# Performance work log

Hardware: AMD Instinct MI355X
Metric: run time of the kernel (lower is better)

The kernel has to match this reference:

```python
import jax, jax.numpy as jnp
import numpy as np

HIDDEN = 1024
HEADS = 16
HEAD_DIM = 64
B, S = 2, 2048
SCALE = 1.0 / np.sqrt(HEAD_DIM)
NEG = -1e9


def setup_inputs() -> dict:
    key = jax.random.key(0)
    k1, k2, k3, k4, k5 = jax.random.split(key, 5)
    hidden_states = jax.random.normal(k1, (B, S, HIDDEN), dtype=jnp.float32)
    # causal additive mask, broadcast over heads: [B, 1, S, S]
    causal = jnp.where(jnp.tril(jnp.ones((S, S), dtype=bool)), 0.0, NEG).astype(jnp.float32)
    attention_mask = jnp.broadcast_to(causal[None, None], (B, 1, S, S))
    std = 1.0 / np.sqrt(HIDDEN)
    Wq = jax.random.normal(k2, (HIDDEN, HEADS * HEAD_DIM), dtype=jnp.float32) * std
    Wk = jax.random.normal(k3, (HIDDEN, HEADS * HEAD_DIM), dtype=jnp.float32) * std
    Wv = jax.random.normal(k4, (HIDDEN, HEADS * HEAD_DIM), dtype=jnp.float32) * std
    Wo = jax.random.normal(k5, (HEADS * HEAD_DIM, HIDDEN), dtype=jnp.float32) * std
    return {"hidden_states": hidden_states, "attention_mask": attention_mask,
            "Wq": Wq, "Wk": Wk, "Wv": Wv, "Wo": Wo}


def reference(hidden_states, attention_mask, Wq, Wk, Wv, Wo):
    b, s, _ = hidden_states.shape
    # projections (eval mode: dropouts are identity)
    q = (hidden_states @ Wq).reshape(b, s, HEADS, HEAD_DIM).transpose(0, 2, 1, 3)  # [B,H,S,D]
    k = (hidden_states @ Wk).reshape(b, s, HEADS, HEAD_DIM).transpose(0, 2, 1, 3)
    v = (hidden_states @ Wv).reshape(b, s, HEADS, HEAD_DIM).transpose(0, 2, 1, 3)
    scores = jnp.einsum('bhqd,bhkd->bhqk', q, k) * SCALE + attention_mask  # [B,H,S,S]
    probs = jax.nn.softmax(scores, axis=-1)
    out = jnp.einsum('bhqk,bhkd->bhqd', probs, v)  # [B,H,S,D]
    out = out.transpose(0, 2, 1, 3).reshape(b, s, HEADS * HEAD_DIM)
    return out @ Wo  # [B,S,HIDDEN]
```

## Files before the change

### kernel.cpp

```cpp
#include <hip/hip_runtime.h>

typedef unsigned short u16;
typedef unsigned int u32;
typedef __bf16 bf16x8 __attribute__((ext_vector_type(8)));
typedef float f32x4 __attribute__((ext_vector_type(4)));

#define MFMA(a, b, c) __builtin_amdgcn_mfma_f32_16x16x32_bf16(a, b, c, 0, 0, 0)

#define GLD16(gsrc, ldst)                                                          \
  __builtin_amdgcn_global_load_lds(                                                \
      (const __attribute__((address_space(1))) void*)(gsrc),                       \
      (__attribute__((address_space(3))) void*)(ldst), 16, 0, 0)

#if __has_builtin(__builtin_amdgcn_exp2f)
#define EXP2(x) __builtin_amdgcn_exp2f(x)
#else
#define EXP2(x) exp2f(x)
#endif

__device__ __forceinline__ u16 f2bf(float f) {
  return __builtin_bit_cast(u16, (__bf16)f);
}

__device__ __forceinline__ u32 pk2(float a, float b) {
  __bf16 x = (__bf16)a, y = (__bf16)b;
  return (u32)__builtin_bit_cast(u16, x) | ((u32)__builtin_bit_cast(u16, y) << 16);
}

__device__ __forceinline__ float bf2f(u16 u) {
  return __builtin_bit_cast(float, ((u32)u) << 16);
}

__global__ __launch_bounds__(256) void k_prep(
    const float* __restrict__ X, const float* __restrict__ Wq,
    const float* __restrict__ Wk, const float* __restrict__ Wv,
    const float* __restrict__ Wo, u16* __restrict__ Xb,
    u16* __restrict__ Wt, u16* __restrict__ Wot) {
  __shared__ u16 t[32][33];
  int bid = blockIdx.x;
  if (bid < 2048) {
    int i = bid * 256 + threadIdx.x;
    const float4* p = (const float4*)X + (size_t)i * 2;
    float4 a = p[0], b = p[1];
    uint4 o;
    o.x = pk2(a.x, a.y);
    o.y = pk2(a.z, a.w);
    o.z = pk2(b.x, b.y);
    o.w = pk2(b.z, b.w);
    *(uint4*)(Xb + (size_t)i * 8) = o;
    return;
  }
  bid -= 2048;
  const int k0 = (bid & 31) * 32, n0 = (bid >> 5) * 32;
  const int x = threadIdx.x & 31, y = threadIdx.x >> 5;
  const float* src = (n0 < 1024) ? Wq : (n0 < 2048) ? Wk : (n0 < 3072) ? Wv : Wo;
  const int ncol = n0 & 1023;
#pragma unroll
  for (int rr = 0; rr < 4; ++rr) {
    int kl = y + rr * 8;
    t[x][kl] = f2bf(src[(size_t)(k0 + kl) * 1024 + ncol + x]);
  }
  __syncthreads();
  u16* dst = (n0 < 3072) ? (Wt + (size_t)n0 * 1024) : (Wot + (size_t)(n0 - 3072) * 1024);
#pragma unroll
  for (int rr = 0; rr < 4; ++rr) {
    int nl = y + rr * 8;
    dst[(size_t)nl * 1024 + k0 + x] = t[nl][x];
  }
}


__global__ __launch_bounds__(256) void k_gemm_qkv(const u16* __restrict__ A_,
                                                  const u16* __restrict__ Bt,
                                                  u16* __restrict__ Q,
                                                  u16* __restrict__ K,
                                                  u16* __restrict__ Vt) {
  __shared__ __align__(16) u16 As[2][128 * 32];
  __shared__ __align__(16) u16 Bs[2][128 * 32];
  const int tid = threadIdx.x;
  const int w = tid >> 6, l = tid & 63;
  const int lr = l & 15, lg = l >> 4;
  const int lin = blockIdx.y * 24 + blockIdx.x;
  const int swz = (lin & 7) * 96 + (lin >> 3);
  const int tM = (swz / 24) * 128, tN = (swz % 24) * 128;
  const int wr = w >> 1, wc = w & 1;
  const int bufsel = tN >> 10;

  const int srow = l >> 2;
  const int scol = (((l & 3) ^ ((l >> 3) & 3)) << 3);
  const u16* Ag = A_ + (size_t)(tM + srow) * 1024 + scol;
  const u16* Bg = Bt + (size_t)(tN + srow) * 1024 + scol;
  const int rs = (lr >> 1) & 3;

#define STAGE_QKV(buf, kk)                                                   \
  {                                                                          \
    GLD16(Ag + (size_t)(w * 16) * 1024 + (kk), &As[buf][(w * 16) * 32]);     \
    GLD16(Ag + (size_t)(64 + w * 16) * 1024 + (kk), &As[buf][(64 + w * 16) * 32]); \
    GLD16(Bg + (size_t)(w * 16) * 1024 + (kk), &Bs[buf][(w * 16) * 32]);     \
    GLD16(Bg + (size_t)(64 + w * 16) * 1024 + (kk), &Bs[buf][(64 + w * 16) * 32]); \
  }

  f32x4 acc[4][4] = {};
  STAGE_QKV(0, 0)
  __syncthreads();
  int cur = 0;

  if (bufsel < 2) {
    for (int t = 0; t < 32; ++t) {
      if (t < 31) STAGE_QKV(cur ^ 1, (t + 1) * 32)
      const u16* Ac = &As[cur][0];
      const u16* Bc = &Bs[cur][0];
      bf16x8 a[4], b[4];
#pragma unroll
      for (int m = 0; m < 4; ++m)
        a[m] = *(const bf16x8*)(Ac + (wr * 64 + m * 16 + lr) * 32 + ((lg ^ rs) << 3));
#pragma unroll
      for (int n = 0; n < 4; ++n)
        b[n] = *(const bf16x8*)(Bc + (wc * 64 + n * 16 + lr) * 32 + ((lg ^ rs) << 3));
#pragma unroll
      for (int m = 0; m < 4; ++m)
#pragma unroll
        for (int n = 0; n < 4; ++n) acc[m][n] = MFMA(b[n], a[m], acc[m][n]);
      __syncthreads();
      cur ^= 1;
    }
    u16* dst = bufsel ? K : Q;
    const float sc = bufsel ? 1.0f : 0.180336880111124f;
#pragma unroll
    for (int m = 0; m < 4; ++m) {
      int s = tM + wr * 64 + m * 16 + lr;
      int b_ = s >> 11, sr2 = s & 2047;
#pragma unroll
      for (int n = 0; n < 4; ++n) {
        int c2 = (tN + wc * 64 + n * 16 + lg * 4) & 1023;
        int h = c2 >> 6, d = c2 & 63;
        uint2 val;
        val.x = pk2(acc[m][n][0] * sc, acc[m][n][1] * sc);
        val.y = pk2(acc[m][n][2] * sc, acc[m][n][3] * sc);
        *(uint2*)(dst + ((size_t)(b_ * 16 + h) * 2048 + sr2) * 64 + d) = val;
      }
    }
  } else {
    for (int t = 0; t < 32; ++t) {
      if (t < 31) STAGE_QKV(cur ^ 1, (t + 1) * 32)
      const u16* Ac = &As[cur][0];
      const u16* Bc = &Bs[cur][0];
      bf16x8 a[4], b[4];
#pragma unroll
      for (int m = 0; m < 4; ++m)
        a[m] = *(const bf16x8*)(Ac + (wr * 64 + m * 16 + lr) * 32 + ((lg ^ rs) << 3));
#pragma unroll
      for (int n = 0; n < 4; ++n)
        b[n] = *(const bf16x8*)(Bc + (wc * 64 + n * 16 + lr) * 32 + ((lg ^ rs) << 3));
#pragma unroll
      for (int m = 0; m < 4; ++m)
#pragma unroll
        for (int n = 0; n < 4; ++n) acc[m][n] = MFMA(a[m], b[n], acc[m][n]);
      __syncthreads();
      cur ^= 1;
    }
#pragma unroll
    for (int m = 0; m < 4; ++m) {
      int r0 = tM + wr * 64 + m * 16 + lg * 4;
      int b_ = r0 >> 11, s0 = r0 & 2047;
#pragma unroll
      for (int n = 0; n < 4; ++n) {
        int c2 = (tN + wc * 64 + n * 16 + lr) & 1023;
        int h = c2 >> 6, d = c2 & 63;
        uint2 val;
        val.x = pk2(acc[m][n][0], acc[m][n][1]);
        val.y = pk2(acc[m][n][2], acc[m][n][3]);
        *(uint2*)(Vt + ((size_t)(b_ * 16 + h) * 64 + d) * 2048 + s0) = val;
      }
    }
  }
#undef STAGE_QKV
}

__global__ __launch_bounds__(256, 4) void k_attn(const u16* __restrict__ Q,
                                                 const u16* __restrict__ Kg,
                                                 const u16* __restrict__ Vtg,
                                                 u16* __restrict__ AO,
                                                 u16* __restrict__ PO,
                                                 float* __restrict__ ML) {
  __shared__ __align__(16) u16 Ks[2][64 * 64];
  __shared__ __align__(16) u16 Vs[2][64 * 64];
  __shared__ __align__(16) u16 Ps[4][16 * 64];
  const int tid = threadIdx.x;
  const int w = tid >> 6, l = tid & 63;
  const int lr = l & 15, lg = l >> 4;

  const int idx = blockIdx.x;
  const int bh = idx & 31;
  const int g = idx >> 5;
  int qt, c0;
  if (g < 16) { qt = 16 + g; c0 = 0; }
  else if (g < 32) { qt = 31 - (g - 16); c0 = 1; }
  else { qt = 15 - (g - 32); c0 = 0; }
  const int nkt = (qt < 16) ? (qt + 1) : (c0 == 0 ? 16 : qt - 15);
  const bool hasdiag = (qt < 16) || (c0 == 1);
  const int q0 = qt * 64;

  const u16* Qp = Q + (size_t)bh * 2048 * 64;
  const u16* Kp = Kg + (size_t)bh * 2048 * 64;
  const u16* Vp = Vtg + (size_t)bh * 64 * 2048;

  const int qrow = q0 + w * 16 + lr;
  bf16x8 qa0 = *(const bf16x8*)(Qp + (size_t)qrow * 64 + lg * 8);
  bf16x8 qa1 = *(const bf16x8*)(Qp + (size_t)qrow * 64 + 32 + lg * 8);

  f32x4 oacc[4] = {};
  float m_run = -1e30f, l_run = 0.f;

  const int srow = l >> 3;
  const int scol = ((l & 7) ^ srow) * 8;
  const int sw = (lr & 7) << 3;

  const u16* kptr = Kp + ((size_t)c0 * 1024 + srow) * 64 + scol;
  const u16* vptr = Vp + (size_t)srow * 2048 + c0 * 1024 + scol;

#pragma unroll
  for (int j = 0; j < 2; ++j) {
    int base = j * 32 + w * 8;
    GLD16(kptr + base * 64, &Ks[0][base * 64]);
    GLD16(vptr + (size_t)base * 2048, &Vs[0][base * 64]);
  }
  kptr += 4096;
  vptr += 64;
  __syncthreads();

  int cur = 0;

#define ATTN_TILE(DOPRE, DOMASK)                                                   \
  {                                                                                \
    if (DOPRE) {                                                                   \
      _Pragma("unroll") for (int j = 0; j < 2; ++j) {                              \
        int base = j * 32 + w * 8;                                                 \
        GLD16(kptr + base * 64, &Ks[cur ^ 1][base * 64]);                          \
        GLD16(vptr + (size_t)base * 2048, &Vs[cur ^ 1][base * 64]);                \
      }                                                                            \
      kptr += 4096;                                                                \
      vptr += 64;                                                                  \
    }                                                                              \
    f32x4 st[4];                                                                   \
    __builtin_amdgcn_s_setprio(1);                                                 \
    _Pragma("unroll") for (int n = 0; n < 4; ++n) {                                \
      const u16* kr = &Ks[cur][(n * 16 + lr) * 64];                                \
      bf16x8 kb0 = *(const bf16x8*)(kr + ((lg << 3) ^ sw));                        \
      bf16x8 kb1 = *(const bf16x8*)(kr + (((4 + lg) << 3) ^ sw));                  \
      f32x4 z = {0.f, 0.f, 0.f, 0.f};                                              \
      z = MFMA(kb0, qa0, z);                                                       \
      z = MFMA(kb1, qa1, z);                                                       \
      st[n] = z;                                                                   \
    }                                                                              \
    __builtin_amdgcn_s_setprio(0);                                                 \
    float mx = -1e30f;                                                             \
    _Pragma("unroll") for (int n = 0; n < 4; ++n)                                  \
        _Pragma("unroll") for (int j = 0; j < 4; ++j) {                            \
      float s = st[n][j];                                                          \
      if (DOMASK && (n * 16 + lg * 4 + j) > (w * 16 + lr)) s = -1e30f;             \
      st[n][j] = s;                                                                \
      mx = fmaxf(mx, s);                                                           \
    }                                                                              \
    mx = fmaxf(mx, __shfl_xor(mx, 16, 64));                                        \
    mx = fmaxf(mx, __shfl_xor(mx, 32, 64));                                        \
    const bool grow = __any(mx > m_run + 8.0f);               \
    float mnew = grow ? fmaxf(m_run, mx) : m_run;                                  \
    float rsum = 0.f;                                                              \
    _Pragma("unroll") for (int n = 0; n < 4; ++n)                                  \
        _Pragma("unroll") for (int j = 0; j < 4; ++j) {                            \
      float p = EXP2(st[n][j] - mnew);                                             \
      st[n][j] = p;                                                                \
      rsum += p;                                                                   \
    }                                                                              \
    rsum += __shfl_xor(rsum, 16, 64);                                              \
    rsum += __shfl_xor(rsum, 32, 64);                                              \
    if (grow) {                                                                    \
      float fsc = EXP2(m_run - mnew);                                              \
      l_run = l_run * fsc + rsum;                                                  \
      m_run = mnew;                                                                \
      _Pragma("unroll") for (int n = 0; n < 4; ++n)                                \
          _Pragma("unroll") for (int j = 0; j < 4; ++j) oacc[n][j] *= fsc;         \
    } else {                                                                       \
      l_run += rsum;                                                               \
    }                                                                              \
    u16* pb = &Ps[w][0];                                                           \
    _Pragma("unroll") for (int n = 0; n < 4; ++n) {                                \
      int slot = n * 2 + (lg >> 1);                                                \
      int off = lr * 64 + ((slot ^ (lr & 7)) << 3) + (lg & 1) * 4;                 \
      uint2 val;                                                                   \
      val.x = pk2(st[n][0], st[n][1]);                                             \
      val.y = pk2(st[n][2], st[n][3]);                                             \
      *(uint2*)(pb + off) = val;                                                   \
    }                                                                              \
    bf16x8 pa0 = *(const bf16x8*)(pb + lr * 64 + ((lg << 3) ^ sw));                \
    bf16x8 pa1 = *(const bf16x8*)(pb + lr * 64 + (((4 + lg) << 3) ^ sw));          \
    __builtin_amdgcn_s_setprio(1);                                                 \
    _Pragma("unroll") for (int n = 0; n < 4; ++n) {                                \
      const u16* vr = &Vs[cur][(n * 16 + lr) * 64];                                \
      bf16x8 vb0 = *(const bf16x8*)(vr + ((lg << 3) ^ sw));                        \
      bf16x8 vb1 = *(const bf16x8*)(vr + (((4 + lg) << 3) ^ sw));                  \
      oacc[n] = MFMA(vb0, pa0, oacc[n]);                                           \
      oacc[n] = MFMA(vb1, pa1, oacc[n]);                                           \
    }                                                                              \
    __builtin_amdgcn_s_setprio(0);                                                 \
  }

  for (int it = 0; it < nkt - 1; ++it) {
    ATTN_TILE(true, false);
    __syncthreads();
    cur ^= 1;
  }
  if (hasdiag) {
    ATTN_TILE(false, true);
  } else {
    ATTN_TILE(false, false);
  }
#undef ATTN_TILE

  if (qt < 16) {
    const int b_ = bh >> 4, h = bh & 15;
    const float linv = 1.0f / l_run;
    const int s = q0 + w * 16 + lr;
    u16* dst = AO + ((size_t)(b_ * 2048 + s)) * 1024 + h * 64 + lg * 4;
#pragma unroll
    for (int n = 0; n < 4; ++n) {
      uint2 val;
      val.x = pk2(oacc[n][0] * linv, oacc[n][1] * linv);
      val.y = pk2(oacc[n][2] * linv, oacc[n][3] * linv);
      *(uint2*)(dst + n * 16) = val;
    }
  } else {
    const int p = (bh * 16 + (qt - 16)) * 2 + c0;
    u16* po = PO + (size_t)p * 4096 + (size_t)(w * 16 + lr) * 64 + lg * 4;
#pragma unroll
    for (int n = 0; n < 4; ++n) {
      uint2 val;
      val.x = pk2(oacc[n][0], oacc[n][1]);
      val.y = pk2(oacc[n][2], oacc[n][3]);
      *(uint2*)(po + n * 16) = val;
    }
    if (lg == 0) {
      ML[(size_t)p * 128 + (w * 16 + lr)] = m_run;
      ML[(size_t)p * 128 + 64 + (w * 16 + lr)] = l_run;
    }
  }
}

__global__ __launch_bounds__(256) void k_combine(const u16* __restrict__ PO,
                                                 const float* __restrict__ ML,
                                                 u16* __restrict__ AO) {
  const int blk = blockIdx.x;
  const int bh = blk >> 4, qt = 16 + (blk & 15);
  const int row = threadIdx.x >> 2;
  const int dseg = (threadIdx.x & 3) * 16;
  const size_t p0 = (size_t)blk * 2;
  const float m0 = ML[p0 * 128 + row], l0 = ML[p0 * 128 + 64 + row];
  const float m1 = ML[p0 * 128 + 128 + row], l1 = ML[p0 * 128 + 192 + row];
  const float M = fmaxf(m0, m1);
  float w0 = EXP2(m0 - M), w1 = EXP2(m1 - M);
  const float inv = 1.0f / (l0 * w0 + l1 * w1);
  w0 *= inv;
  w1 *= inv;
  const u16* o0 = PO + p0 * 4096 + (size_t)row * 64 + dseg;
  const u16* o1 = o0 + 4096;
  const int b_ = bh >> 4, h = bh & 15;
  u16* dst = AO + ((size_t)(b_ * 2048 + qt * 64 + row)) * 1024 + h * 64 + dseg;
#pragma unroll
  for (int half = 0; half < 2; ++half) {
    uint4 a = *(const uint4*)(o0 + half * 8);
    uint4 b = *(const uint4*)(o1 + half * 8);
    u32 aw[4] = {a.x, a.y, a.z, a.w};
    u32 bw[4] = {b.x, b.y, b.z, b.w};
    uint4 o;
    u32 ow[4];
#pragma unroll
    for (int i = 0; i < 4; ++i) {
      float r0 = bf2f((u16)(aw[i] & 0xffffu)) * w0 + bf2f((u16)(bw[i] & 0xffffu)) * w1;
      float r1 = bf2f((u16)(aw[i] >> 16)) * w0 + bf2f((u16)(bw[i] >> 16)) * w1;
      ow[i] = pk2(r0, r1);
    }
    o.x = ow[0]; o.y = ow[1]; o.z = ow[2]; o.w = ow[3];
    *(uint4*)(dst + half * 8) = o;
  }
}

__global__ __launch_bounds__(256) void k_gemm_out(const u16* __restrict__ A_,
                                                  const u16* __restrict__ Bt,
                                                  float* __restrict__ out) {
  __shared__ __align__(16) u16 As[2][128 * 32];
  __shared__ __align__(16) u16 Bs[2][64 * 32];
  const int tid = threadIdx.x;
  const int w = tid >> 6, l = tid & 63;
  const int lr = l & 15, lg = l >> 4;
  const int lin = blockIdx.y * 16 + blockIdx.x;
  const int swz = (lin & 7) * 64 + (lin >> 3);
  const int tM = (swz / 16) * 128, tN = (swz % 16) * 64;

  const int srow = l >> 2;
  const int scol = (((l & 3) ^ ((l >> 3) & 3)) << 3);
  const u16* Ag = A_ + (size_t)(tM + srow) * 1024 + scol;
  const u16* Bg = Bt + (size_t)(tN + srow) * 1024 + scol;
  const int rs = (lr >> 1) & 3;

#define STAGE_OUT(buf, kk)                                                   \
  {                                                                          \
    GLD16(Ag + (size_t)(w * 16) * 1024 + (kk), &As[buf][(w * 16) * 32]);     \
    GLD16(Ag + (size_t)(64 + w * 16) * 1024 + (kk), &As[buf][(64 + w * 16) * 32]); \
    GLD16(Bg + (size_t)(w * 16) * 1024 + (kk), &Bs[buf][(w * 16) * 32]);     \
  }

  f32x4 acc[2][4] = {};
  STAGE_OUT(0, 0)
  __syncthreads();
  int cur = 0;
  for (int t = 0; t < 32; ++t) {
    if (t < 31) STAGE_OUT(cur ^ 1, (t + 1) * 32)
    const u16* Ac = &As[cur][0];
    const u16* Bc = &Bs[cur][0];
    bf16x8 a[2], b[4];
#pragma unroll
    for (int m = 0; m < 2; ++m)
      a[m] = *(const bf16x8*)(Ac + (w * 32 + m * 16 + lr) * 32 + ((lg ^ rs) << 3));
#pragma unroll
    for (int n = 0; n < 4; ++n)
      b[n] = *(const bf16x8*)(Bc + (n * 16 + lr) * 32 + ((lg ^ rs) << 3));
#pragma unroll
    for (int m = 0; m < 2; ++m)
#pragma unroll
      for (int n = 0; n < 4; ++n) acc[m][n] = MFMA(b[n], a[m], acc[m][n]);
    __syncthreads();
    cur ^= 1;
  }
#undef STAGE_OUT

#pragma unroll
  for (int m = 0; m < 2; ++m) {
    int s = tM + w * 32 + m * 16 + lr;
#pragma unroll
    for (int n = 0; n < 4; ++n) {
      int c = tN + n * 16 + lg * 4;
      float4 v;
      v.x = acc[m][n][0];
      v.y = acc[m][n][1];
      v.z = acc[m][n][2];
      v.w = acc[m][n][3];
      *(float4*)(out + (size_t)s * 1024 + c) = v;
    }
  }
}

extern "C" void kernel_launch(void* const* d_in, const int* in_sizes, int n_in,
                              void* d_out, int out_size, void* d_ws, size_t ws_size,
                              hipStream_t stream) {
  const float* X = (const float*)d_in[0];
  const float* Wq = (const float*)d_in[2];
  const float* Wk = (const float*)d_in[3];
  const float* Wv = (const float*)d_in[4];
  const float* Wo = (const float*)d_in[5];
  float* out = (float*)d_out;

  char* ws = (char*)d_ws;
  if (ws_size < (size_t)48 * 1024 * 1024) return;
  u16* Xb  = (u16*)(ws);
  u16* Wt  = (u16*)(ws + 8388608);
  u16* Wot = (u16*)(ws + 14680064);
  u16* Q   = (u16*)(ws + 16777216);
  u16* K   = (u16*)(ws + 25165824);
  u16* Vt  = (u16*)(ws + 33554432);
  u16* AO  = (u16*)(ws + 41943040);
  u16*   PO = (u16*)(ws);
  float* ML = (float*)(ws + 8388608);

  k_prep<<<6144, 256, 0, stream>>>(X, Wq, Wk, Wv, Wo, Xb, Wt, Wot);
  k_gemm_qkv<<<dim3(24, 32), 256, 0, stream>>>(Xb, Wt, Q, K, Vt);
  k_attn<<<1536, 256, 0, stream>>>(Q, K, Vt, AO, PO, ML);
  k_combine<<<512, 256, 0, stream>>>(PO, ML, AO);
  k_gemm_out<<<dim3(16, 32), 256, 0, stream>>>(AO, Wot, out);
}
```

Measured before the change: 117.3 us.

## Halve attention KV tile to 32 keys to raise occupancy to six waves

Shrinks the K/V LDS tiles in the attention kernel from 64 keys to 32 and doubles the number of KV iterations. This lowers shared-memory use and registers per block so the launch bound can rise to 6 blocks per CU for better latency hiding. The LDS swizzles and P-tile layout are reworked to match, and the causal mask is now applied to the last two tiles using absolute positions. In exchange there are twice as many barriers and softmax rescale steps, and less MFMA work per iteration. The last two tiles are always masked, even for blocks that have no diagonal tile.

```diff
diff --git a/kernel.cpp b/kernel.cpp
--- a/kernel.cpp
+++ b/kernel.cpp
@@ -177,15 +177,15 @@
 #undef STAGE_QKV
 }
 
-__global__ __launch_bounds__(256, 4) void k_attn(const u16* __restrict__ Q,
+__global__ __launch_bounds__(256, 6) void k_attn(const u16* __restrict__ Q,
                                                  const u16* __restrict__ Kg,
                                                  const u16* __restrict__ Vtg,
                                                  u16* __restrict__ AO,
                                                  u16* __restrict__ PO,
                                                  float* __restrict__ ML) {
-  __shared__ __align__(16) u16 Ks[2][64 * 64];
-  __shared__ __align__(16) u16 Vs[2][64 * 64];
-  __shared__ __align__(16) u16 Ps[4][16 * 64];
+  __shared__ __align__(16) u16 Ks[2][32 * 64];
+  __shared__ __align__(16) u16 Vs[2][64 * 32];
+  __shared__ __align__(16) u16 Ps[4][16 * 32];
   const int tid = threadIdx.x;
   const int w = tid >> 6, l = tid & 63;
   const int lr = l & 15, lg = l >> 4;
@@ -197,8 +197,7 @@
   if (g < 16) { qt = 16 + g; c0 = 0; }
   else if (g < 32) { qt = 31 - (g - 16); c0 = 1; }
   else { qt = 15 - (g - 32); c0 = 0; }
-  const int nkt = (qt < 16) ? (qt + 1) : (c0 == 0 ? 16 : qt - 15);
-  const bool hasdiag = (qt < 16) || (c0 == 1);
+  const int nkt = (qt < 16) ? (2 * qt + 2) : (c0 == 0 ? 32 : 2 * (qt - 15));
   const int q0 = qt * 64;
 
   const u16* Qp = Q + (size_t)bh * 2048 * 64;
@@ -212,39 +211,34 @@
   f32x4 oacc[4] = {};
   float m_run = -1e30f, l_run = 0.f;
 
-  const int srow = l >> 3;
-  const int scol = ((l & 7) ^ srow) * 8;
+  const int srk = l >> 3;
+  const int sck = ((l & 7) ^ srk) * 8;
+  const int scv = (((l & 3) ^ ((l >> 3) & 3)) << 3);
   const int sw = (lr & 7) << 3;
-
-  const u16* kptr = Kp + ((size_t)c0 * 1024 + srow) * 64 + scol;
-  const u16* vptr = Vp + (size_t)srow * 2048 + c0 * 1024 + scol;
-
-#pragma unroll
-  for (int j = 0; j < 2; ++j) {
-    int base = j * 32 + w * 8;
-    GLD16(kptr + base * 64, &Ks[0][base * 64]);
-    GLD16(vptr + (size_t)base * 2048, &Vs[0][base * 64]);
-  }
-  kptr += 4096;
-  vptr += 64;
+  const int sv = ((lr >> 1) & 3) << 3;
+
+  const u16* kptr = Kp + ((size_t)c0 * 1024 + w * 8 + srk) * 64 + sck;
+  const u16* vptr = Vp + (size_t)(w * 16 + (l >> 2)) * 2048 + c0 * 1024 + scv;
+
+  GLD16(kptr, &Ks[0][(w * 8) * 64]);
+  GLD16(vptr, &Vs[0][(w * 16) * 32]);
+  kptr += 2048;
+  vptr += 32;
   __syncthreads();
 
   int cur = 0;
 
-#define ATTN_TILE(DOPRE, DOMASK)                                                   \
+#define ATTN_TILE(DOPRE, DOMASK, KVB)                                              \
   {                                                                                \
     if (DOPRE) {                                                                   \
-      _Pragma("unroll") for (int j = 0; j < 2; ++j) {                              \
-        int base = j * 32 + w * 8;                                                 \
-        GLD16(kptr + base * 64, &Ks[cur ^ 1][base * 64]);                          \
-        GLD16(vptr + (size_t)base * 2048, &Vs[cur ^ 1][base * 64]);                \
-      }                                                                            \
-      kptr += 4096;                                                                \
-      vptr += 64;                                                                  \
-    }                                                                              \
-    f32x4 st[4];                                                                   \
+      GLD16(kptr, &Ks[cur ^ 1][(w * 8) * 64]);                                     \
+      GLD16(vptr, &Vs[cur ^ 1][(w * 16) * 32]);                                    \
+      kptr += 2048;                                                                \
+      vptr += 32;                                                                  \
+    }                                                                              \
+    f32x4 st[2];                                                                   \
     __builtin_amdgcn_s_setprio(1);                                                 \
-    _Pragma("unroll") for (int n = 0; n < 4; ++n) {                                \
+    _Pragma("unroll") for (int n = 0; n < 2; ++n) {                                \
       const u16* kr = &Ks[cur][(n * 16 + lr) * 64];                                \
       bf16x8 kb0 = *(const bf16x8*)(kr + ((lg << 3) ^ sw));                        \
       bf16x8 kb1 = *(const bf16x8*)(kr + (((4 + lg) << 3) ^ sw));                  \
@@ -255,10 +249,10 @@
     }                                                                              \
     __builtin_amdgcn_s_setprio(0);                                                 \
     float mx = -1e30f;                                                             \
-    _Pragma("unroll") for (int n = 0; n < 4; ++n)                                  \
+    _Pragma("unroll") for (int n = 0; n < 2; ++n)                                  \
         _Pragma("unroll") for (int j = 0; j < 4; ++j) {                            \
       float s = st[n][j];                                                          \
-      if (DOMASK && (n * 16 + lg * 4 + j) > (w * 16 + lr)) s = -1e30f;             \
+      if (DOMASK && ((KVB) + n * 16 + lg * 4 + j) > (q0 + w * 16 + lr)) s = -1e30f; \
       st[n][j] = s;                                                                \
       mx = fmaxf(mx, s);                                                           \
     }                                                                              \
@@ -267,7 +261,7 @@
     const bool grow = __any(mx > m_run + 8.0f);               \
     float mnew = grow ? fmaxf(m_run, mx) : m_run;                                  \
     float rsum = 0.f;                                                              \
-    _Pragma("unroll") for (int n = 0; n < 4; ++n)                                  \
+    _Pragma("unroll") for (int n = 0; n < 2; ++n)                                  \
         _Pragma("unroll") for (int j = 0; j < 4; ++j) {                            \
       float p = EXP2(st[n][j] - mnew);                                             \
       st[n][j] = p;                                                                \
@@ -285,36 +279,34 @@
       l_run += rsum;                                                               \
     }                                                                              \
     u16* pb = &Ps[w][0];                                                           \
-    _Pragma("unroll") for (int n = 0; n < 4; ++n) {                                \
-      int slot = n * 2 + (lg >> 1);                                                \
-      int off = lr * 64 + ((slot ^ (lr & 7)) << 3) + (lg & 1) * 4;                 \
-      uint2 val;                                                                   \
-      val.x = pk2(st[n][0], st[n][1]);                                             \
-      val.y = pk2(st[n][2], st[n][3]);                                             \
-      *(uint2*)(pb + off) = val;                                                   \
-    }                                                                              \
-    bf16x8 pa0 = *(const bf16x8*)(pb + lr * 64 + ((lg << 3) ^ sw));                \
-    bf16x8 pa1 = *(const bf16x8*)(pb + lr * 64 + (((4 + lg) << 3) ^ sw));          \
+    _Pragma("unroll") for (int n = 0; n < 2; ++n)                                  \
+        _Pragma("unroll") for (int jh = 0; jh < 2; ++jh) {                         \
+      u32 v = pk2(st[n][2 * jh], st[n][2 * jh + 1]);                               \
+      int gq = (n * 2 + (lg >> 1)) ^ ((lr >> 1) & 3);                              \
+      *(u32*)(pb + lr * 32 + gq * 8 + ((lg * 2 + jh) & 3) * 2) = v;                \
+    }                                                                              \
+    bf16x8 pa0 = *(const bf16x8*)(pb + lr * 32 + ((lg << 3) ^ sv));                \
     __builtin_amdgcn_s_setprio(1);                                                 \
     _Pragma("unroll") for (int n = 0; n < 4; ++n) {                                \
-      const u16* vr = &Vs[cur][(n * 16 + lr) * 64];                                \
-      bf16x8 vb0 = *(const bf16x8*)(vr + ((lg << 3) ^ sw));                        \
-      bf16x8 vb1 = *(const bf16x8*)(vr + (((4 + lg) << 3) ^ sw));                  \
-      oacc[n] = MFMA(vb0, pa0, oacc[n]);                                           \
-      oacc[n] = MFMA(vb1, pa1, oacc[n]);                                           \
+      const u16* vr = &Vs[cur][(n * 16 + lr) * 32];                                \
+      bf16x8 vb = *(const bf16x8*)(vr + ((lg << 3) ^ sv));                         \
+      oacc[n] = MFMA(vb, pa0, oacc[n]);                                            \
     }                                                                              \
     __builtin_amdgcn_s_setprio(0);                                                 \
   }
 
-  for (int it = 0; it < nkt - 1; ++it) {
-    ATTN_TILE(true, false);
+  for (int it = 0; it < nkt - 2; ++it) {
+    ATTN_TILE(true, false, 0);
     __syncthreads();
     cur ^= 1;
   }
-  if (hasdiag) {
-    ATTN_TILE(false, true);
-  } else {
-    ATTN_TILE(false, false);
+  {
+    ATTN_TILE(true, true, (c0 * 1024 + (nkt - 2) * 32));
+    __syncthreads();
+    cur ^= 1;
+  }
+  {
+    ATTN_TILE(false, true, (c0 * 1024 + (nkt - 1) * 32));
   }
 #undef ATTN_TILE
 
```

Result: slower. 122.9 us (+4.7%).

## Feed P to PV MFMA from registers, permute V reads to match

Applied to the files above, without the earlier changes.

Removes the per-wave LDS round trip for the probability tile. The packed P values in the QK score layout are used directly as the MFMA A/B operand, and the V loads from shared memory are reindexed into 8-byte pieces so the k-dimension order matches. It also defers the cross-lane row-sum reduction to once after the loop, keeping only per-lane partial sums (the max is still reduced each tile). Occupancy hint goes from 4 to 5 blocks per CU because the Ps buffer is gone. In exchange, each PV step issues more, smaller LDS reads.

```diff
diff --git a/kernel.cpp b/kernel.cpp
--- a/kernel.cpp
+++ b/kernel.cpp
@@ -4,6 +4,7 @@
 typedef unsigned int u32;
 typedef __bf16 bf16x8 __attribute__((ext_vector_type(8)));
 typedef float f32x4 __attribute__((ext_vector_type(4)));
+typedef u32 u32x4 __attribute__((ext_vector_type(4)));
 
 #define MFMA(a, b, c) __builtin_amdgcn_mfma_f32_16x16x32_bf16(a, b, c, 0, 0, 0)
 
@@ -177,7 +178,7 @@
 #undef STAGE_QKV
 }
 
-__global__ __launch_bounds__(256, 4) void k_attn(const u16* __restrict__ Q,
+__global__ __launch_bounds__(256, 5) void k_attn(const u16* __restrict__ Q,
                                                  const u16* __restrict__ Kg,
                                                  const u16* __restrict__ Vtg,
                                                  u16* __restrict__ AO,
@@ -185,7 +186,6 @@
                                                  float* __restrict__ ML) {
   __shared__ __align__(16) u16 Ks[2][64 * 64];
   __shared__ __align__(16) u16 Vs[2][64 * 64];
-  __shared__ __align__(16) u16 Ps[4][16 * 64];
   const int tid = threadIdx.x;
   const int w = tid >> 6, l = tid & 63;
   const int lr = l & 15, lg = l >> 4;
@@ -215,6 +215,9 @@
   const int srow = l >> 3;
   const int scol = ((l & 7) ^ srow) * 8;
   const int sw = (lr & 7) << 3;
+  const int vr7 = lr & 7;
+  const int vh = (lg & 1) * 4;
+  const int g0 = lg >> 1;
 
   const u16* kptr = Kp + ((size_t)c0 * 1024 + srow) * 64 + scol;
   const u16* vptr = Vp + (size_t)srow * 2048 + c0 * 1024 + scol;
@@ -273,8 +276,6 @@
       st[n][j] = p;                                                                \
       rsum += p;                                                                   \
     }                                                                              \
-    rsum += __shfl_xor(rsum, 16, 64);                                              \
-    rsum += __shfl_xor(rsum, 32, 64);                                              \
     if (grow) {                                                                    \
       float fsc = EXP2(m_run - mnew);                                              \
       l_run = l_run * fsc + rsum;                                                  \
@@ -284,24 +285,30 @@
     } else {                                                                       \
       l_run += rsum;                                                               \
     }                                                                              \
-    u16* pb = &Ps[w][0];                                                           \
-    _Pragma("unroll") for (int n = 0; n < 4; ++n) {                                \
-      int slot = n * 2 + (lg >> 1);                                                \
-      int off = lr * 64 + ((slot ^ (lr & 7)) << 3) + (lg & 1) * 4;                 \
-      uint2 val;                                                                   \
-      val.x = pk2(st[n][0], st[n][1]);                                             \
-      val.y = pk2(st[n][2], st[n][3]);                                             \
-      *(uint2*)(pb + off) = val;                                                   \
-    }                                                                              \
-    bf16x8 pa0 = *(const bf16x8*)(pb + lr * 64 + ((lg << 3) ^ sw));                \
-    bf16x8 pa1 = *(const bf16x8*)(pb + lr * 64 + (((4 + lg) << 3) ^ sw));          \
+      \
+    u32x4 tp0, tp1;                                                                \
+    tp0.x = pk2(st[0][0], st[0][1]);                                               \
+    tp0.y = pk2(st[0][2], st[0][3]);                                               \
+    tp0.z = pk2(st[1][0], st[1][1]);                                               \
+    tp0.w = pk2(st[1][2], st[1][3]);                                               \
+    tp1.x = pk2(st[2][0], st[2][1]);                                               \
+    tp1.y = pk2(st[2][2], st[2][3]);                                               \
+    tp1.z = pk2(st[3][0], st[3][1]);                                               \
+    tp1.w = pk2(st[3][2], st[3][3]);                                               \
+    bf16x8 pa0 = __builtin_bit_cast(bf16x8, tp0);                                  \
+    bf16x8 pa1 = __builtin_bit_cast(bf16x8, tp1);                                  \
     __builtin_amdgcn_s_setprio(1);                                                 \
     _Pragma("unroll") for (int n = 0; n < 4; ++n) {                                \
       const u16* vr = &Vs[cur][(n * 16 + lr) * 64];                                \
-      bf16x8 vb0 = *(const bf16x8*)(vr + ((lg << 3) ^ sw));                        \
-      bf16x8 vb1 = *(const bf16x8*)(vr + (((4 + lg) << 3) ^ sw));                  \
-      oacc[n] = MFMA(vb0, pa0, oacc[n]);                                           \
-      oacc[n] = MFMA(vb1, pa1, oacc[n]);                                           \
+      uint2 v00 = *(const uint2*)(vr + (((g0 ^ vr7) << 3) + vh));                  \
+      uint2 v01 = *(const uint2*)(vr + ((((2 + g0) ^ vr7) << 3) + vh));            \
+      uint2 v10 = *(const uint2*)(vr + ((((4 + g0) ^ vr7) << 3) + vh));            \
+      uint2 v11 = *(const uint2*)(vr + ((((6 + g0) ^ vr7) << 3) + vh));            \
+      u32x4 tv0, tv1;                                                              \
+      tv0.x = v00.x; tv0.y = v00.y; tv0.z = v01.x; tv0.w = v01.y;                  \
+      tv1.x = v10.x; tv1.y = v10.y; tv1.z = v11.x; tv1.w = v11.y;                  \
+      oacc[n] = MFMA(__builtin_bit_cast(bf16x8, tv0), pa0, oacc[n]);               \
+      oacc[n] = MFMA(__builtin_bit_cast(bf16x8, tv1), pa1, oacc[n]);               \
     }                                                                              \
     __builtin_amdgcn_s_setprio(0);                                                 \
   }
@@ -318,9 +325,13 @@
   }
 #undef ATTN_TILE
 
+  float lsum = l_run;
+  lsum += __shfl_xor(lsum, 16, 64);
+  lsum += __shfl_xor(lsum, 32, 64);
+
   if (qt < 16) {
     const int b_ = bh >> 4, h = bh & 15;
-    const float linv = 1.0f / l_run;
+    const float linv = 1.0f / lsum;
     const int s = q0 + w * 16 + lr;
     u16* dst = AO + ((size_t)(b_ * 2048 + s)) * 1024 + h * 64 + lg * 4;
 #pragma unroll
@@ -342,7 +353,7 @@
     }
     if (lg == 0) {
       ML[(size_t)p * 128 + (w * 16 + lr)] = m_run;
-      ML[(size_t)p * 128 + 64 + (w * 16 + lr)] = l_run;
+      ML[(size_t)p * 128 + 64 + (w * 16 + lr)] = lsum;
     }
   }
 }
```

New measurement: 123.8 us. 1.06x slower.
